# Kernel optimization log

Measured on AMD Instinct MI355X. Metric: run time of the kernel, lower is better.

The kernel has to match this reference:

```python
import jax, jax.numpy as jnp
import numpy as np

L, D, H, N, R = 4, 256, 512, 16, 8  # layers, d_model, hidden=2*d_model, state_dim, dt_rank
OUT_LEN, IN_DIM = 96, 32
EPS = 1e-5


def _layernorm(v, g, b):
    m = jnp.mean(v, axis=-1, keepdims=True)
    var = jnp.mean((v - m) ** 2, axis=-1, keepdims=True)
    return (v - m) / jnp.sqrt(var + EPS) * g + b


def _pos_encoding(T, d):
    pos = jnp.arange(T, dtype=jnp.float32)[:, None]
    div = jnp.exp(jnp.arange(0, d, 2, dtype=jnp.float32) * (-np.log(10000.0) / d))
    pe = jnp.zeros((T, d), dtype=jnp.float32)
    pe = pe.at[:, 0::2].set(jnp.sin(pos * div))
    pe = pe.at[:, 1::2].set(jnp.cos(pos * div))
    return pe


def setup_inputs() -> dict:
    key = jax.random.key(0)
    ks = jax.random.split(key, 20)
    inp = {
        "x": jax.random.normal(ks[0], (8, 1024, IN_DIM), dtype=jnp.float32),
        "emb_w": jax.random.normal(ks[1], (D, IN_DIM), dtype=jnp.float32) * 0.1,
        "emb_b": jnp.zeros((D,), dtype=jnp.float32),
        "norm_g": jnp.ones((L, D), dtype=jnp.float32),
        "norm_b": jnp.zeros((L, D), dtype=jnp.float32),
        "in_w": jax.random.normal(ks[2], (L, H, D), dtype=jnp.float32) * (1.0 / np.sqrt(D)),
        "conv_w": jax.random.normal(ks[3], (L, H, 1, 3), dtype=jnp.float32) * 0.5,
        "A_p": jax.random.normal(ks[4], (L, H, N), dtype=jnp.float32) * 0.01,
        "D_p": jnp.ones((L, H), dtype=jnp.float32),
        "dt1_w": jax.random.normal(ks[5], (L, R, H), dtype=jnp.float32) * (1.0 / np.sqrt(H)),
        "dt1_b": jnp.zeros((L, R), dtype=jnp.float32),
        "dt2_w": jax.random.normal(ks[6], (L, H, R), dtype=jnp.float32) * (1.0 / np.sqrt(R)),
        "dt2_b": jnp.zeros((L, H), dtype=jnp.float32),
        "out_w": jax.random.normal(ks[7], (L, D, H), dtype=jnp.float32) * (1.0 / np.sqrt(H)),
        "final_g": jnp.ones((D,), dtype=jnp.float32),
        "final_b": jnp.zeros((D,), dtype=jnp.float32),
        "head1_w": jax.random.normal(ks[8], (D, D), dtype=jnp.float32) * (1.0 / np.sqrt(D)),
        "head1_b": jnp.zeros((D,), dtype=jnp.float32),
        "head2_w": jax.random.normal(ks[9], (OUT_LEN, D), dtype=jnp.float32) * (1.0 / np.sqrt(D)),
        "head2_b": jnp.zeros((OUT_LEN,), dtype=jnp.float32),
    }
    return inp


def _mamba_block(h, g, b, in_w, conv_w, A_p, D_p, dt1_w, dt1_b, dt2_w, dt2_b, out_w):
    res = h
    v = _layernorm(h, g, b)            # [B,T,D]
    v = jnp.einsum('btd,hd->bth', v, in_w)  # [B,T,H]
    # depthwise conv1d, kernel 3, padding 1, groups=H
    vc = jnp.transpose(v, (0, 2, 1))   # [B,H,T]
    vc = jax.lax.conv_general_dilated(vc, conv_w, window_strides=(1,),
                                      padding=[(1, 1)], feature_group_count=H,
                                      dimension_numbers=('NCH', 'OIH', 'NCH'))
    v = jnp.transpose(jax.nn.silu(vc), (0, 2, 1))  # [B,T,H]
    dt = jax.nn.relu(jnp.einsum('bth,rh->btr', v, dt1_w) + dt1_b)
    dt = jnp.einsum('btr,hr->bth', dt, dt2_w) + dt2_b
    dt = jax.nn.softplus(dt)           # [B,T,H]
    A = -jnp.exp(A_p)                  # [H,N]
    safe_A = jnp.where(jnp.abs(A) < 1e-5, jnp.ones_like(A), A)

    B_sz = v.shape[0]
    state0 = jnp.zeros((B_sz, H, N), dtype=v.dtype)

    def step(state, inp):
        x_t, dt_t = inp  # [B,H] each
        dA = A * dt_t[..., None]            # [B,H,N]
        discA = jnp.exp(dA)
        discB = (discA - 1.0) / safe_A * dt_t[..., None]
        state = discA * state + discB * x_t[..., None]
        y = jnp.einsum('bhn,hn->bh', state, A_p) + D_p * x_t
        return state, y

    xs = (jnp.transpose(v, (1, 0, 2)), jnp.transpose(dt, (1, 0, 2)))  # [T,B,H]
    _, ys = jax.lax.scan(step, state0, xs)
    y = jnp.transpose(ys, (1, 0, 2))   # [B,T,H]
    return res + jnp.einsum('bth,dh->btd', y, out_w)


def reference(x, emb_w, emb_b, norm_g, norm_b, in_w, conv_w, A_p, D_p,
              dt1_w, dt1_b, dt2_w, dt2_b, out_w, final_g, final_b,
              head1_w, head1_b, head2_w, head2_b):
    h = jnp.einsum('bti,di->btd', x, emb_w) + emb_b  # [B,T,D]
    h = h + _pos_encoding(h.shape[1], D)[None]
    for l in range(L):
        h = _mamba_block(h, norm_g[l], norm_b[l], in_w[l], conv_w[l], A_p[l],
                         D_p[l], dt1_w[l], dt1_b[l], dt2_w[l], dt2_b[l], out_w[l])
    h = _layernorm(h, final_g, final_b)
    h = h[:, -1, :]                    # last token [B,D]
    h = jax.nn.silu(h @ head1_w.T + head1_b)
    return h @ head2_w.T + head2_b     # [B, OUT_LEN]
```

## Files before the change

kernel.cpp:

```cpp
#include <hip/hip_runtime.h>
#include <hip/hip_bf16.h>
#include <math.h>

#define BB 8
#define TT 1024
#define DD 256
#define HH 512
#define NN 16
#define RR 8
#define OUT_LEN 96
#define IN_DIM 32
#define MM (BB*TT)

#define SC 16
#define CC (TT/SC)

typedef unsigned short u16;
typedef unsigned int u32;
typedef __attribute__((ext_vector_type(8))) short short8;
typedef __attribute__((ext_vector_type(8))) unsigned short u16x8;
typedef __attribute__((ext_vector_type(4))) float float4v;

__device__ __forceinline__ u16 f2bf(float f) {
    __hip_bfloat16 h = __float2bfloat16(f);
    return *(u16*)&h;
}
__device__ __forceinline__ float bf2f(u16 u) {
    u32 v = ((u32)u) << 16;
    return *(float*)&v;
}

#define GLD_LDS16(src, dst) __builtin_amdgcn_global_load_lds( \
    (const __attribute__((address_space(1))) void*)(src),     \
    (__attribute__((address_space(3))) void*)(dst), 16, 0, 0)

#define SBAR()   asm volatile("s_barrier" ::: "memory")
#define VMCNT0() asm volatile("s_waitcnt vmcnt(0)" ::: "memory")
#define VMCNT4() asm volatile("s_waitcnt vmcnt(4)" ::: "memory")
#define VMCNT6() asm volatile("s_waitcnt vmcnt(6)" ::: "memory")
#define VMCNT8() asm volatile("s_waitcnt vmcnt(8)" ::: "memory")

__global__ __launch_bounds__(256) void embed_ln_cvt_kernel(
    const float* __restrict__ x, const float* __restrict__ emb_w,
    const float* __restrict__ emb_b,
    const float* __restrict__ g, const float* __restrict__ b,
    float* __restrict__ h, u16* __restrict__ lnout,
    const float* __restrict__ w_in, u16* __restrict__ wbf_in,
    const float* __restrict__ w_out, u16* __restrict__ wbf_out, int nw)
{
    int bid = blockIdx.x;
    if (bid >= MM) {
        int i = (bid - MM) * 256 + threadIdx.x;
        if (i < nw) wbf_in[i] = f2bf(w_in[i]);
        else        wbf_out[i - nw] = f2bf(w_out[i - nw]);
        return;
    }

    int bt = bid;
    int d  = threadIdx.x;
    int t  = bt & (TT - 1);

    __shared__ float xs[IN_DIM];
    __shared__ float red[4], red2[4];
    if (threadIdx.x < IN_DIM) xs[threadIdx.x] = x[bt * IN_DIM + threadIdx.x];
    __syncthreads();

    const float* w = emb_w + d * IN_DIM;
    float acc = emb_b[d];
#pragma unroll
    for (int i = 0; i < IN_DIM; i++) acc = fmaf(xs[i], w[i], acc);

    int i2 = d & ~1;
    float div = __expf(-(float)i2 * 0.0359778918f);
    float arg = (float)t * div;
    float pe = (d & 1) ? __cosf(arg) : __sinf(arg);
    float val = acc + pe;
    h[bt * DD + d] = val;

    float s = val;
#pragma unroll
    for (int o = 32; o > 0; o >>= 1) s += __shfl_down(s, o);
    int lane = d & 63, wave = d >> 6;
    if (lane == 0) red[wave] = s;
    __syncthreads();
    float mean = (red[0] + red[1] + red[2] + red[3]) * (1.0f / DD);

    float c = val - mean;
    float s2 = c * c;
#pragma unroll
    for (int o = 32; o > 0; o >>= 1) s2 += __shfl_down(s2, o);
    if (lane == 0) red2[wave] = s2;
    __syncthreads();
    float var = (red2[0] + red2[1] + red2[2] + red2[3]) * (1.0f / DD);

    lnout[bt * DD + d] = f2bf(c * rsqrtf(var + 1e-5f) * g[d] + b[d]);
}

template<int BM, int BN, int OUT_BF16>
__global__ __launch_bounds__(256) void gemm_bf16(
    const u16* __restrict__ A, const u16* __restrict__ B,
    void* __restrict__ Cv, int M, int N, int K, int addC)
{
    constexpr int BK = 64;
    constexpr int MT = BM / 32;
    constexpr int NT = BN / 32;
    static_assert(BM == 128 && BN == 64, "vmcnt count assumes 6 loads/thread");

    __shared__ __align__(16) u16 Al[2][8][BM][8];
    __shared__ __align__(16) u16 Bl[2][8][BN][8];

    const int tid = threadIdx.x;
    const int bm = blockIdx.y * BM;
    const int bn = blockIdx.x * BN;
    const int wid = tid >> 6, lane = tid & 63;
    const int wm = wid >> 1, wn = wid & 1;
    const int lq = lane >> 4, lm = lane & 15;

    float4v acc[MT][NT];
#pragma unroll
    for (int i = 0; i < MT; i++)
#pragma unroll
        for (int j = 0; j < NT; j++) acc[i][j] = (float4v){0.f, 0.f, 0.f, 0.f};

#pragma unroll
    for (int it = 0; it < (8 * BM) / 256; it++) {
        int c = it * 256 + tid;
        int q = c / BM, row = c % BM;
        GLD_LDS16(A + (size_t)(bm + row) * K + q * 8, &Al[0][q][row][0]);
    }
#pragma unroll
    for (int it = 0; it < (8 * BN) / 256; it++) {
        int c = it * 256 + tid;
        int q = c / BN, row = c % BN;
        GLD_LDS16(B + (size_t)(bn + row) * K + q * 8, &Bl[0][q][row][0]);
    }

    const int nt = K / BK;
    int cur = 0;
    for (int i = 0; i < nt; i++) {
        if (i + 1 < nt) {
            int nxt = cur ^ 1;
            int k1 = (i + 1) * BK;
#pragma unroll
            for (int it = 0; it < (8 * BM) / 256; it++) {
                int c = it * 256 + tid;
                int q = c / BM, row = c % BM;
                GLD_LDS16(A + (size_t)(bm + row) * K + k1 + q * 8, &Al[nxt][q][row][0]);
            }
#pragma unroll
            for (int it = 0; it < (8 * BN) / 256; it++) {
                int c = it * 256 + tid;
                int q = c / BN, row = c % BN;
                GLD_LDS16(B + (size_t)(bn + row) * K + k1 + q * 8, &Bl[nxt][q][row][0]);
            }
            VMCNT6();
        } else {
            VMCNT0();
        }
        SBAR();

        short8 af[2][MT], bf[2][NT];
#pragma unroll
        for (int kk = 0; kk < 2; kk++) {
#pragma unroll
            for (int mt = 0; mt < MT; mt++)
                af[kk][mt] = *(const short8*)&Al[cur][kk * 4 + lq][wm * (BM / 2) + mt * 16 + lm][0];
#pragma unroll
            for (int nt2 = 0; nt2 < NT; nt2++)
                bf[kk][nt2] = *(const short8*)&Bl[cur][kk * 4 + lq][wn * (BN / 2) + nt2 * 16 + lm][0];
        }

#pragma unroll
        for (int kk = 0; kk < 2; kk++)
#pragma unroll
            for (int mt = 0; mt < MT; mt++)
#pragma unroll
                for (int nt2 = 0; nt2 < NT; nt2++)
                    acc[mt][nt2] = __builtin_amdgcn_mfma_f32_16x16x32_bf16(
                        af[kk][mt], bf[kk][nt2], acc[mt][nt2], 0, 0, 0);
        SBAR();
        cur ^= 1;
    }

#pragma unroll
    for (int mt = 0; mt < MT; mt++)
#pragma unroll
        for (int nt2 = 0; nt2 < NT; nt2++) {
            int row0 = bm + wm * (BM / 2) + mt * 16 + lq * 4;
            int col  = bn + wn * (BN / 2) + nt2 * 16 + lm;
#pragma unroll
            for (int r = 0; r < 4; r++) {
                float vv = acc[mt][nt2][r];
                if (OUT_BF16) {
                    ((u16*)Cv)[(size_t)(row0 + r) * N + col] = f2bf(vv);
                } else {
                    float* cp = (float*)Cv + (size_t)(row0 + r) * N + col;
                    if (addC) vv += *cp;
                    *cp = vv;
                }
            }
        }
}

__device__ __forceinline__ float softplus_f(float s) {
    return (s > 20.0f) ? s : __logf(1.0f + __expf(s));
}

__global__ __launch_bounds__(512, 4) void conv_scan1(
    const u16* __restrict__ vbf, const float* __restrict__ cwg,
    const float* __restrict__ w1g, const float* __restrict__ b1g,
    const float* __restrict__ dt2_w, const float* __restrict__ dt2_b,
    const float* __restrict__ A_p,
    u16* __restrict__ vsb, float* __restrict__ dtr,
    u16* __restrict__ Lst, float* __restrict__ sdt)
{
    const int c = blockIdx.x;
    const int b = blockIdx.y;
    const int tid = threadIdx.x;
    const int wave = tid >> 6, lane = tid & 63;
    const int h0 = lane * 8;

    __shared__ float w1s[RR * 2 * 256];
    __shared__ u16   a_lds[SC][HH];
    __shared__ float ds[SC * RR];

#pragma unroll
    for (int i = 0; i < 2; i++) {
        int rci = wave + i * 8;
        int r = rci >> 1, jc = rci & 1;
        float4 wv = *(const float4*)(w1g + r * HH + lane * 8 + jc * 4);
        *(float4*)&w1s[rci * 256 + lane * 4] = wv;
    }
    __syncthreads();

    const float* wp = cwg + h0 * 3;
#pragma unroll
    for (int i = 0; i < 2; i++) {
        int tr = wave + i * 8;
        int t  = c * SC + tr;
        size_t m = (size_t)b * TT + t;

        const u16* vrow = vbf + m * HH + h0;
        u16x8 x0 = *(const u16x8*)vrow;
        u16x8 xm = (t > 0)      ? *(const u16x8*)(vrow - HH) : (u16x8)(0);
        u16x8 xp = (t < TT - 1) ? *(const u16x8*)(vrow + HH) : (u16x8)(0);

        float a[8];
        u16x8 o;
#pragma unroll
        for (int j = 0; j < 8; j++) {
            float s = wp[j * 3] * bf2f(xm[j]);
            s = fmaf(wp[j * 3 + 1], bf2f(x0[j]), s);
            s = fmaf(wp[j * 3 + 2], bf2f(xp[j]), s);
            s = s / (1.0f + __expf(-s));
            a[j] = s;
            o[j] = f2bf(s);
        }
        *(u16x8*)(vsb + m * HH + h0) = o;
        *(u16x8*)&a_lds[tr][h0]      = o;

        float acc[RR];
#pragma unroll
        for (int r = 0; r < RR; r++) {
            float4 wlo = *(const float4*)&w1s[(r * 2 + 0) * 256 + lane * 4];
            float4 whi = *(const float4*)&w1s[(r * 2 + 1) * 256 + lane * 4];
            float s = a[0] * wlo.x;
            s = fmaf(a[1], wlo.y, s);
            s = fmaf(a[2], wlo.z, s);
            s = fmaf(a[3], wlo.w, s);
            s = fmaf(a[4], whi.x, s);
            s = fmaf(a[5], whi.y, s);
            s = fmaf(a[6], whi.z, s);
            s = fmaf(a[7], whi.w, s);
            acc[r] = s;
        }
#pragma unroll
        for (int r = 0; r < RR; r++) {
#pragma unroll
            for (int o2 = 1; o2 < 64; o2 <<= 1) acc[r] += __shfl_xor(acc[r], o2);
        }
        if (lane == 0) {
#pragma unroll
            for (int r = 0; r < RR; r++) acc[r] = fmaxf(acc[r] + b1g[r], 0.0f);
            *(float4*)(dtr + m * RR)     = make_float4(acc[0], acc[1], acc[2], acc[3]);
            *(float4*)(dtr + m * RR + 4) = make_float4(acc[4], acc[5], acc[6], acc[7]);
#pragma unroll
            for (int r = 0; r < RR; r++) ds[tr * RR + r] = acc[r];
        }
    }
    __syncthreads();

    const int h = tid;
    float A2[NN], invA[NN], st[NN];
    const float* ap = A_p + h * NN;
#pragma unroll
    for (int n = 0; n < NN; n++) {
        float av = -__expf(ap[n]);
        A2[n] = av * 1.44269504f;
        invA[n] = 1.0f / av;
        st[n] = 0.0f;
    }
    float w2[RR];
#pragma unroll
    for (int r = 0; r < RR; r++) w2[r] = dt2_w[h * RR + r];
    float b2 = dt2_b[h];

    float xv = bf2f(a_lds[0][h]);
    float s_dt = 0.0f;
#pragma unroll 2
    for (int t = 0; t < SC; t++) {
        float xn = (t + 1 < SC) ? bf2f(a_lds[t + 1][h]) : 0.0f;
        float s = b2;
#pragma unroll
        for (int r = 0; r < RR; r++) s = fmaf(ds[t * RR + r], w2[r], s);
        float dt = softplus_f(s);
        s_dt += dt;
        float dtx = dt * xv;
#pragma unroll
        for (int n = 0; n < NN; n++) {
            float e = __builtin_amdgcn_exp2f(A2[n] * dt);
            float u = invA[n] * dtx;
            st[n] = fmaf(e, st[n] + u, -u);
        }
        xv = xn;
    }

    size_t base = (((size_t)c * BB + b) * HH + h) * NN;
    u16x8 lo, hi;
#pragma unroll
    for (int n = 0; n < 8; n++) { lo[n] = f2bf(st[n]); hi[n] = f2bf(st[n + 8]); }
    *(u16x8*)(Lst + base)     = lo;
    *(u16x8*)(Lst + base + 8) = hi;
    sdt[((size_t)c * BB + b) * HH + h] = s_dt;
}

__global__ __launch_bounds__(256) void scan_carry_par(
    const float* __restrict__ A_p, const float* __restrict__ sdt,
    u16* __restrict__ Lst)
{
    int gw   = (blockIdx.x << 2) | (threadIdx.x >> 6);
    int lane = threadIdx.x & 63;
    int b = gw >> 9;
    int h = gw & 511;

    size_t sidx = ((size_t)lane * BB + b) * HH + h;
    float sd = sdt[sidx];
    const float* ap = A_p + h * NN;
    u16x8 Llo = *(const u16x8*)(Lst + sidx * NN);
    u16x8 Lhi = *(const u16x8*)(Lst + sidx * NN + 8);
    u16x8 Elo, Ehi;
#pragma unroll
    for (int n = 0; n < NN; n++) {
        float An = -__expf(ap[n]);
        float p  = __expf(An * sd);
        float lv = bf2f((n < 8) ? Llo[n] : Lhi[n - 8]);
#pragma unroll
        for (int d2 = 1; d2 < 64; d2 <<= 1) {
            float pp = __shfl_up(p, d2);
            float pl = __shfl_up(lv, d2);
            if (lane >= d2) { lv = fmaf(pl, p, lv); p = pp * p; }
        }
        float E = __shfl_up(lv, 1);
        if (lane == 0) E = 0.0f;
        if (n < 8) Elo[n] = f2bf(E); else Ehi[n - 8] = f2bf(E);
    }
    *(u16x8*)(Lst + sidx * NN)     = Elo;
    *(u16x8*)(Lst + sidx * NN + 8) = Ehi;
}

__global__ __launch_bounds__(512) void scan2_gemm2_ln(
    const u16* __restrict__ vsb, const float* __restrict__ dtr,
    const float* __restrict__ dt2_w, const float* __restrict__ dt2_b,
    const float* __restrict__ A_p, const float* __restrict__ D_p,
    const u16* __restrict__ carry,
    const u16* __restrict__ B,
    float* __restrict__ h,
    const float* __restrict__ g, const float* __restrict__ bb,
    u16* __restrict__ lnout, int doLN,
    const float* __restrict__ w1h, const float* __restrict__ b1h,
    const float* __restrict__ w2h, const float* __restrict__ b2h,
    float* __restrict__ outp, int doHead)
{
    const int bid = blockIdx.x;
    const int b   = bid >> 5;
    const int tb  = bid & 31;
    const int t0  = tb * 32;
    const int c0  = tb * 2;
    const int bm  = bid * 32;

    const int tid = threadIdx.x;
    const int wid = tid >> 6;
    const int lane = tid & 63;
    const int lq = lane >> 4, lm = lane & 15;
    const int wm = wid >> 2;
    const int wn = wid & 3;

    __shared__ __align__(16) u16 Yl[32 * 512];
    __shared__ __align__(16) u16 Bl[3][8][256][8];
    __shared__ float ds[32 * RR];
    __shared__ float rs[4][32], qs[4][32];
    __shared__ float hn[DD], sl1[DD];

#pragma unroll
    for (int pt = 0; pt < 2; pt++) {
#pragma unroll
        for (int it = 0; it < 4; it++) {
            int cth = it * 512 + tid;
            int q = cth >> 8, row = cth & 255;
            GLD_LDS16(B + (size_t)row * 512 + pt * 64 + q * 8, &Bl[pt][q][row][0]);
        }
    }

    const int hh = tid;

    const u16* vb0 = vsb + ((size_t)b * TT + (size_t)(c0 + 0) * SC) * HH + hh;
    const u16* vb1 = vsb + ((size_t)b * TT + (size_t)(c0 + 1) * SC) * HH + hh;
    u16 xr0[SC], xr1[SC];
#pragma unroll
    for (int t = 0; t < SC; t++) xr0[t] = vb0[(size_t)t * HH];
#pragma unroll
    for (int t = 0; t < SC; t++) xr1[t] = vb1[(size_t)t * HH];

    float st0[NN], st1[NN];
    {
        size_t cb0 = (((size_t)(c0 + 0) * BB + b) * HH + hh) * NN;
        size_t cb1 = (((size_t)(c0 + 1) * BB + b) * HH + hh) * NN;
        u16x8 l0 = *(const u16x8*)(carry + cb0);
        u16x8 h0 = *(const u16x8*)(carry + cb0 + 8);
        u16x8 l1 = *(const u16x8*)(carry + cb1);
        u16x8 h1 = *(const u16x8*)(carry + cb1 + 8);
#pragma unroll
        for (int n = 0; n < 8; n++) {
            st0[n] = bf2f(l0[n]); st0[n + 8] = bf2f(h0[n]);
            st1[n] = bf2f(l1[n]); st1[n + 8] = bf2f(h1[n]);
        }
    }

    if (tid < 256) {
        int tr = tid >> 3, r = tid & 7;
        ds[tid] = dtr[((size_t)b * TT + t0 + tr) * RR + r];
    }

    float A2[NN], invA[NN], Ap[NN], w2[RR];
    const float* ap = A_p + hh * NN;
#pragma unroll
    for (int n = 0; n < NN; n++) {
        float apv = ap[n]; Ap[n] = apv;
        float a = -__expf(apv);
        A2[n] = a * 1.44269504f; invA[n] = 1.0f / a;
    }
#pragma unroll
    for (int r = 0; r < RR; r++) w2[r] = dt2_w[hh * RR + r];
    float b2 = dt2_b[hh];
    float Dp = D_p[hh];
    __syncthreads();

#pragma unroll
    for (int t = 0; t < SC; t++) {
        float s0 = b2, s1 = b2;
#pragma unroll
        for (int r = 0; r < RR; r++) {
            s0 = fmaf(ds[t * RR + r], w2[r], s0);
            s1 = fmaf(ds[(SC + t) * RR + r], w2[r], s1);
        }
        float dt0 = softplus_f(s0);
        float dt1 = softplus_f(s1);
        float xv0 = bf2f(xr0[t]);
        float xv1 = bf2f(xr1[t]);
        float dtx0 = dt0 * xv0, dtx1 = dt1 * xv1;
        float acc0 = Dp * xv0,  acc1 = Dp * xv1;
#pragma unroll
        for (int n = 0; n < NN; n++) {
            float e0 = __builtin_amdgcn_exp2f(A2[n] * dt0);
            float u0 = invA[n] * dtx0;
            st0[n] = fmaf(e0, st0[n] + u0, -u0);
            acc0 = fmaf(st0[n], Ap[n], acc0);
            float e1 = __builtin_amdgcn_exp2f(A2[n] * dt1);
            float u1 = invA[n] * dtx1;
            st1[n] = fmaf(e1, st1[n] + u1, -u1);
            acc1 = fmaf(st1[n], Ap[n], acc1);
        }
        Yl[t * 512 + (hh ^ ((t & 7) << 3))] = f2bf(acc0);
        int tr1 = SC + t;
        Yl[tr1 * 512 + (hh ^ ((tr1 & 7) << 3))] = f2bf(acc1);
    }
    __syncthreads();

    float4v acc4[4];
#pragma unroll
    for (int j = 0; j < 4; j++) acc4[j] = (float4v){0.f, 0.f, 0.f, 0.f};

    for (int i = 0; i < 8; i++) {
        if (i + 2 < 8) {
            int nb = (i + 2) % 3;
            int k1 = (i + 2) * 64;
#pragma unroll
            for (int it = 0; it < 4; it++) {
                int cth = it * 512 + tid;
                int q = cth >> 8, row = cth & 255;
                GLD_LDS16(B + (size_t)row * 512 + k1 + q * 8, &Bl[nb][q][row][0]);
            }
            VMCNT8();
        } else if (i + 1 < 8) {
            VMCNT4();
        } else {
            VMCNT0();
        }
        SBAR();

        int cur = i % 3;
        int k0 = i * 64;
        short8 af[2], bf[2][4];
#pragma unroll
        for (int kk = 0; kk < 2; kk++) {
            int row = wm * 16 + lm;
            int kg  = (k0 >> 3) + kk * 4 + lq;
            af[kk] = *(const short8*)&Yl[row * 512 + ((kg ^ (row & 7)) << 3)];
#pragma unroll
            for (int nt = 0; nt < 4; nt++)
                bf[kk][nt] = *(const short8*)&Bl[cur][kk * 4 + lq][wn * 64 + nt * 16 + lm][0];
        }
#pragma unroll
        for (int kk = 0; kk < 2; kk++)
#pragma unroll
            for (int nt = 0; nt < 4; nt++)
                acc4[nt] = __builtin_amdgcn_mfma_f32_16x16x32_bf16(
                    af[kk], bf[kk][nt], acc4[nt], 0, 0, 0);
        SBAR();
    }

    float val[4][4];
    float s1[4] = {0.f, 0.f, 0.f, 0.f}, s2[4] = {0.f, 0.f, 0.f, 0.f};
#pragma unroll
    for (int r = 0; r < 4; r++) {
        int row = bm + wm * 16 + lq * 4 + r;
#pragma unroll
        for (int nt = 0; nt < 4; nt++) {
            int col = wn * 64 + nt * 16 + lm;
            float v = acc4[nt][r] + h[(size_t)row * DD + col];
            val[r][nt] = v;
            s1[r] += v;
            s2[r] = fmaf(v, v, s2[r]);
            h[(size_t)row * DD + col] = v;
        }
    }
#pragma unroll
    for (int r = 0; r < 4; r++) {
#pragma unroll
        for (int o = 1; o < 16; o <<= 1) {
            s1[r] += __shfl_xor(s1[r], o);
            s2[r] += __shfl_xor(s2[r], o);
        }
    }
    if (lm == 0) {
#pragma unroll
        for (int r = 0; r < 4; r++) {
            rs[wn][wm * 16 + lq * 4 + r] = s1[r];
            qs[wn][wm * 16 + lq * 4 + r] = s2[r];
        }
    }
    __syncthreads();

    if (doLN) {
#pragma unroll
        for (int r = 0; r < 4; r++) {
            int i = wm * 16 + lq * 4 + r;
            int row = bm + i;
            float mean = (rs[0][i] + rs[1][i] + rs[2][i] + rs[3][i]) * (1.0f / DD);
            float var  = (qs[0][i] + qs[1][i] + qs[2][i] + qs[3][i]) * (1.0f / DD) - mean * mean;
            float rstd = rsqrtf(var + 1e-5f);
#pragma unroll
            for (int nt = 0; nt < 4; nt++) {
                int col = wn * 64 + nt * 16 + lm;
                lnout[(size_t)row * DD + col] =
                    f2bf((val[r][nt] - mean) * rstd * g[col] + bb[col]);
            }
        }
    }

    if (doHead && tb == 31) {
        const int i31 = 31;
        float mean = (rs[0][i31] + rs[1][i31] + rs[2][i31] + rs[3][i31]) * (1.0f / DD);
        float var  = (qs[0][i31] + qs[1][i31] + qs[2][i31] + qs[3][i31]) * (1.0f / DD) - mean * mean;
        float rstd = rsqrtf(var + 1e-5f);
        const size_t row = (size_t)bm + 31;

        if (tid < DD) {
            float v = h[row * DD + tid];
            hn[tid] = (v - mean) * rstd * g[tid] + bb[tid];
        }
        __syncthreads();

        if (tid < DD) {
            float a1 = b1h[tid];
            const float* w1r = w1h + tid * DD;
#pragma unroll 8
            for (int k = 0; k < DD; k++) a1 = fmaf(hn[k], w1r[k], a1);
            sl1[tid] = a1 / (1.0f + __expf(-a1));
        }
        __syncthreads();

        if (tid < OUT_LEN) {
            float a2 = b2h[tid];
            const float* w2r = w2h + tid * DD;
#pragma unroll 8
            for (int k = 0; k < DD; k++) a2 = fmaf(sl1[k], w2r[k], a2);
            outp[b * OUT_LEN + tid] = a2;
        }
    }
}

extern "C" void kernel_launch(void* const* d_in, const int* in_sizes, int n_in,
                              void* d_out, int out_size, void* d_ws, size_t ws_size,
                              hipStream_t stream)
{
    (void)in_sizes; (void)n_in; (void)out_size; (void)ws_size;

    const float* x       = (const float*)d_in[0];
    const float* emb_w   = (const float*)d_in[1];
    const float* emb_b   = (const float*)d_in[2];
    const float* norm_g  = (const float*)d_in[3];
    const float* norm_b  = (const float*)d_in[4];
    const float* in_w    = (const float*)d_in[5];
    const float* conv_w  = (const float*)d_in[6];
    const float* A_p     = (const float*)d_in[7];
    const float* D_p     = (const float*)d_in[8];
    const float* dt1_w   = (const float*)d_in[9];
    const float* dt1_b   = (const float*)d_in[10];
    const float* dt2_w   = (const float*)d_in[11];
    const float* dt2_b   = (const float*)d_in[12];
    const float* out_w   = (const float*)d_in[13];
    const float* final_g = (const float*)d_in[14];
    const float* final_b = (const float*)d_in[15];
    const float* head1_w = (const float*)d_in[16];
    const float* head1_b = (const float*)d_in[17];
    const float* head2_w = (const float*)d_in[18];
    const float* head2_b = (const float*)d_in[19];
    float* outp = (float*)d_out;

    char* ws = (char*)d_ws;
    float* h     = (float*)ws;                ws += (size_t)MM * DD * 4;
    u16*   vbf   = (u16*)ws;                  ws += (size_t)MM * HH * 2;
    u16*   vsb   = (u16*)ws;                  ws += (size_t)MM * HH * 2;
    u16*   lnbuf = (u16*)ws;                  ws += (size_t)MM * DD * 2;
    float* dtr   = (float*)ws;                ws += (size_t)MM * RR * 4;
    u16*   Lst   = (u16*)ws;                  ws += (size_t)CC * BB * HH * NN * 2;
    float* sdt   = (float*)ws;                ws += (size_t)CC * BB * HH * 4;
    u16*   wbf_in  = (u16*)ws;                ws += (size_t)4 * HH * DD * 2;
    u16*   wbf_out = (u16*)ws;                ws += (size_t)4 * DD * HH * 2;

    const int NW = 4 * HH * DD;
    embed_ln_cvt_kernel<<<MM + (2 * NW) / 256, 256, 0, stream>>>(
        x, emb_w, emb_b, norm_g, norm_b, h, lnbuf,
        in_w, wbf_in, out_w, wbf_out, NW);

    for (int l = 0; l < 4; l++) {
        gemm_bf16<128, 64, 1><<<dim3(HH / 64, MM / 128), 256, 0, stream>>>(
            lnbuf, wbf_in + (size_t)l * HH * DD, vbf, MM, HH, DD, 0);

        conv_scan1<<<dim3(CC, BB), 512, 0, stream>>>(
            vbf, conv_w + (size_t)l * HH * 3,
            dt1_w + (size_t)l * RR * HH, dt1_b + l * RR,
            dt2_w + (size_t)l * HH * RR, dt2_b + l * HH,
            A_p + (size_t)l * HH * NN,
            vsb, dtr, Lst, sdt);

        scan_carry_par<<<(BB * HH) / 4, 256, 0, stream>>>(
            A_p + (size_t)l * HH * NN, sdt, Lst);

        const float* g_next = (l < 3) ? (norm_g + (l + 1) * DD) : final_g;
        const float* b_next = (l < 3) ? (norm_b + (l + 1) * DD) : final_b;
        scan2_gemm2_ln<<<MM / 32, 512, 0, stream>>>(
            vsb, dtr, dt2_w + (size_t)l * HH * RR, dt2_b + l * HH,
            A_p + (size_t)l * HH * NN, D_p + l * HH,
            Lst, wbf_out + (size_t)l * DD * HH,
            h, g_next, b_next, lnbuf, (l < 3) ? 1 : 0,
            head1_w, head1_b, head2_w, head2_b, outp, (l == 3) ? 1 : 0);
    }
}
```

Measured before the change: 470.1 us.

## Emit local scan outputs in first pass and apply carry correction in second

The first scan pass now also computes each chunk's zero-initial-state output y (including the D skip term) and writes it to a new bf16 buffer. The second pass no longer reruns the full recurrence. It adds a carry correction, the sum over n of A_p*carry*exp(A*cumulative dt), using the linearity of the scan. This removes the state-update work from the second kernel but adds a global write and read of an MM×HH bf16 buffer. It also adds rounding, since y is stored in bf16 before the correction is added.

```diff
diff --git a/kernel.cpp b/kernel.cpp
--- a/kernel.cpp
+++ b/kernel.cpp
@@ -210,9 +210,10 @@
     const u16* __restrict__ vbf, const float* __restrict__ cwg,
     const float* __restrict__ w1g, const float* __restrict__ b1g,
     const float* __restrict__ dt2_w, const float* __restrict__ dt2_b,
-    const float* __restrict__ A_p,
+    const float* __restrict__ A_p, const float* __restrict__ D_p,
     u16* __restrict__ vsb, float* __restrict__ dtr,
-    u16* __restrict__ Lst, float* __restrict__ sdt)
+    u16* __restrict__ Lst, float* __restrict__ sdt,
+    u16* __restrict__ ybf)
 {
     const int c = blockIdx.x;
     const int b = blockIdx.y;
@@ -291,11 +292,13 @@
     __syncthreads();
 
     const int h = tid;
-    float A2[NN], invA[NN], st[NN];
+    float A2[NN], invA[NN], Apr[NN], st[NN];
     const float* ap = A_p + h * NN;
 #pragma unroll
     for (int n = 0; n < NN; n++) {
-        float av = -__expf(ap[n]);
+        float apv = ap[n];
+        Apr[n] = apv;
+        float av = -__expf(apv);
         A2[n] = av * 1.44269504f;
         invA[n] = 1.0f / av;
         st[n] = 0.0f;
@@ -304,6 +307,9 @@
 #pragma unroll
     for (int r = 0; r < RR; r++) w2[r] = dt2_w[h * RR + r];
     float b2 = dt2_b[h];
+    float Dp = D_p[h];
+
+    u16* ybase = ybf + ((size_t)b * TT + (size_t)c * SC) * HH + h;
 
     float xv = bf2f(a_lds[0][h]);
     float s_dt = 0.0f;
@@ -316,12 +322,15 @@
         float dt = softplus_f(s);
         s_dt += dt;
         float dtx = dt * xv;
+        float accY = Dp * xv;
 #pragma unroll
         for (int n = 0; n < NN; n++) {
             float e = __builtin_amdgcn_exp2f(A2[n] * dt);
             float u = invA[n] * dtx;
             st[n] = fmaf(e, st[n] + u, -u);
-        }
+            accY = fmaf(st[n], Apr[n], accY);
+        }
+        ybase[(size_t)t * HH] = f2bf(accY);
         xv = xn;
     }
 
@@ -369,9 +378,9 @@
 }
 
 __global__ __launch_bounds__(512) void scan2_gemm2_ln(
-    const u16* __restrict__ vsb, const float* __restrict__ dtr,
+    const u16* __restrict__ ybf, const float* __restrict__ dtr,
     const float* __restrict__ dt2_w, const float* __restrict__ dt2_b,
-    const float* __restrict__ A_p, const float* __restrict__ D_p,
+    const float* __restrict__ A_p,
     const u16* __restrict__ carry,
     const u16* __restrict__ B,
     float* __restrict__ h,
@@ -413,15 +422,8 @@
 
     const int hh = tid;
 
-    const u16* vb0 = vsb + ((size_t)b * TT + (size_t)(c0 + 0) * SC) * HH + hh;
-    const u16* vb1 = vsb + ((size_t)b * TT + (size_t)(c0 + 1) * SC) * HH + hh;
-    u16 xr0[SC], xr1[SC];
-#pragma unroll
-    for (int t = 0; t < SC; t++) xr0[t] = vb0[(size_t)t * HH];
-#pragma unroll
-    for (int t = 0; t < SC; t++) xr1[t] = vb1[(size_t)t * HH];
-
-    float st0[NN], st1[NN];
+    float K0[NN], K1[NN];
+    float A2[NN];
     {
         size_t cb0 = (((size_t)(c0 + 0) * BB + b) * HH + hh) * NN;
         size_t cb1 = (((size_t)(c0 + 1) * BB + b) * HH + hh) * NN;
@@ -429,10 +431,16 @@
         u16x8 h0 = *(const u16x8*)(carry + cb0 + 8);
         u16x8 l1 = *(const u16x8*)(carry + cb1);
         u16x8 h1 = *(const u16x8*)(carry + cb1 + 8);
-#pragma unroll
-        for (int n = 0; n < 8; n++) {
-            st0[n] = bf2f(l0[n]); st0[n + 8] = bf2f(h0[n]);
-            st1[n] = bf2f(l1[n]); st1[n + 8] = bf2f(h1[n]);
+        const float* ap = A_p + hh * NN;
+#pragma unroll
+        for (int n = 0; n < NN; n++) {
+            float apv = ap[n];
+            float av = -__expf(apv);
+            A2[n] = av * 1.44269504f;
+            float c0v = bf2f((n < 8) ? l0[n] : h0[n - 8]);
+            float c1v = bf2f((n < 8) ? l1[n] : h1[n - 8]);
+            K0[n] = apv * c0v;
+            K1[n] = apv * c1v;
         }
     }
 
@@ -441,20 +449,15 @@
         ds[tid] = dtr[((size_t)b * TT + t0 + tr) * RR + r];
     }
 
-    float A2[NN], invA[NN], Ap[NN], w2[RR];
-    const float* ap = A_p + hh * NN;
-#pragma unroll
-    for (int n = 0; n < NN; n++) {
-        float apv = ap[n]; Ap[n] = apv;
-        float a = -__expf(apv);
-        A2[n] = a * 1.44269504f; invA[n] = 1.0f / a;
-    }
+    float w2[RR];
 #pragma unroll
     for (int r = 0; r < RR; r++) w2[r] = dt2_w[hh * RR + r];
     float b2 = dt2_b[hh];
-    float Dp = D_p[hh];
-    __syncthreads();
-
+    __syncthreads();
+
+    const u16* yb0 = ybf + ((size_t)b * TT + (size_t)(c0 + 0) * SC) * HH + hh;
+    const u16* yb1 = ybf + ((size_t)b * TT + (size_t)(c0 + 1) * SC) * HH + hh;
+    float cd0 = 0.0f, cd1 = 0.0f;
 #pragma unroll
     for (int t = 0; t < SC; t++) {
         float s0 = b2, s1 = b2;
@@ -463,26 +466,19 @@
             s0 = fmaf(ds[t * RR + r], w2[r], s0);
             s1 = fmaf(ds[(SC + t) * RR + r], w2[r], s1);
         }
-        float dt0 = softplus_f(s0);
-        float dt1 = softplus_f(s1);
-        float xv0 = bf2f(xr0[t]);
-        float xv1 = bf2f(xr1[t]);
-        float dtx0 = dt0 * xv0, dtx1 = dt1 * xv1;
-        float acc0 = Dp * xv0,  acc1 = Dp * xv1;
+        cd0 += softplus_f(s0);
+        cd1 += softplus_f(s1);
+        float yl0 = bf2f(yb0[(size_t)t * HH]);
+        float yl1 = bf2f(yb1[(size_t)t * HH]);
+        float corr0 = 0.0f, corr1 = 0.0f;
 #pragma unroll
         for (int n = 0; n < NN; n++) {
-            float e0 = __builtin_amdgcn_exp2f(A2[n] * dt0);
-            float u0 = invA[n] * dtx0;
-            st0[n] = fmaf(e0, st0[n] + u0, -u0);
-            acc0 = fmaf(st0[n], Ap[n], acc0);
-            float e1 = __builtin_amdgcn_exp2f(A2[n] * dt1);
-            float u1 = invA[n] * dtx1;
-            st1[n] = fmaf(e1, st1[n] + u1, -u1);
-            acc1 = fmaf(st1[n], Ap[n], acc1);
-        }
-        Yl[t * 512 + (hh ^ ((t & 7) << 3))] = f2bf(acc0);
+            corr0 = fmaf(K0[n], __builtin_amdgcn_exp2f(A2[n] * cd0), corr0);
+            corr1 = fmaf(K1[n], __builtin_amdgcn_exp2f(A2[n] * cd1), corr1);
+        }
+        Yl[t * 512 + (hh ^ ((t & 7) << 3))] = f2bf(yl0 + corr0);
         int tr1 = SC + t;
-        Yl[tr1 * 512 + (hh ^ ((tr1 & 7) << 3))] = f2bf(acc1);
+        Yl[tr1 * 512 + (hh ^ ((tr1 & 7) << 3))] = f2bf(yl1 + corr1);
     }
     __syncthreads();
 
@@ -642,6 +638,7 @@
     float* h     = (float*)ws;                ws += (size_t)MM * DD * 4;
     u16*   vbf   = (u16*)ws;                  ws += (size_t)MM * HH * 2;
     u16*   vsb   = (u16*)ws;                  ws += (size_t)MM * HH * 2;
+    u16*   ybf   = (u16*)ws;                  ws += (size_t)MM * HH * 2;
     u16*   lnbuf = (u16*)ws;                  ws += (size_t)MM * DD * 2;
     float* dtr   = (float*)ws;                ws += (size_t)MM * RR * 4;
     u16*   Lst   = (u16*)ws;                  ws += (size_t)CC * BB * HH * NN * 2;
@@ -662,8 +659,8 @@
             vbf, conv_w + (size_t)l * HH * 3,
             dt1_w + (size_t)l * RR * HH, dt1_b + l * RR,
             dt2_w + (size_t)l * HH * RR, dt2_b + l * HH,
-            A_p + (size_t)l * HH * NN,
-            vsb, dtr, Lst, sdt);
+            A_p + (size_t)l * HH * NN, D_p + l * HH,
+            vsb, dtr, Lst, sdt, ybf);
 
         scan_carry_par<<<(BB * HH) / 4, 256, 0, stream>>>(
             A_p + (size_t)l * HH * NN, sdt, Lst);
@@ -671,8 +668,8 @@
         const float* g_next = (l < 3) ? (norm_g + (l + 1) * DD) : final_g;
         const float* b_next = (l < 3) ? (norm_b + (l + 1) * DD) : final_b;
         scan2_gemm2_ln<<<MM / 32, 512, 0, stream>>>(
-            vsb, dtr, dt2_w + (size_t)l * HH * RR, dt2_b + l * HH,
-            A_p + (size_t)l * HH * NN, D_p + l * HH,
+            ybf, dtr, dt2_w + (size_t)l * HH * RR, dt2_b + l * HH,
+            A_p + (size_t)l * HH * NN,
             Lst, wbf_out + (size_t)l * DD * HH,
             h, g_next, b_next, lnbuf, (l < 3) ? 1 : 0,
             head1_w, head1_b, head2_w, head2_b, outp, (l == 3) ? 1 : 0);
```

New measurement: 453.1 us. 1.04x faster.
